# Kernel tuning notes

Measured on AMD Instinct MI355X. Metric: run time of the kernel, lower is better.

The kernel has to match this reference:

```python
import jax, jax.numpy as jnp
import numpy as np
from jax import lax

EPS = 1e-5


def binarize(x):
    return jnp.sign(x)


def conv3x3(x, w):
    # x: NCHW, w: OIHW, stride 1, padding 1 (SAME for k=3)
    return lax.conv_general_dilated(
        x, w, window_strides=(1, 1), padding=((1, 1), (1, 1)),
        dimension_numbers=("NCHW", "OIHW", "NCHW"))


def prelu(x, a):
    # a broadcastable per-channel slope
    return jnp.where(x >= 0, x, a * x)


def bn(x, gamma, beta, axes):
    mean = jnp.mean(x, axis=axes, keepdims=True)
    var = jnp.var(x, axis=axes, keepdims=True)
    shp = [1] * x.ndim
    shp[1] = x.shape[1]
    g = gamma.reshape(shp)
    b = beta.reshape(shp)
    return (x - mean) * lax.rsqrt(var + EPS) * g + b


def setup_inputs() -> dict:
    key = jax.random.key(0)
    ks = jax.random.split(key, 8)
    B = 256
    C = [1, 64, 128]
    FC_IN = 28 * 28 * C[-1]  # 100352
    F1, F2 = 1024, 10
    inp = {
        "x": jax.random.normal(ks[0], (B, C[0], 28, 28), jnp.float32),
        "cw0": jax.random.normal(ks[1], (C[1], C[0], 3, 3), jnp.float32) * 0.1,
        "cp0": jnp.full((C[1],), 0.25, jnp.float32),
        "cg0": jnp.ones((C[1],), jnp.float32),
        "cb0": jnp.zeros((C[1],), jnp.float32),
        "cw1": jax.random.normal(ks[2], (C[2], C[1], 3, 3), jnp.float32) * 0.1,
        "cp1": jnp.full((C[2],), 0.25, jnp.float32),
        "cg1": jnp.ones((C[2],), jnp.float32),
        "cb1": jnp.zeros((C[2],), jnp.float32),
        "fw0": jax.random.normal(ks[3], (F1, FC_IN), jnp.float32) * 0.02,
        "fp0": jnp.full((F1,), 0.25, jnp.float32),
        "fg0": jnp.ones((F1,), jnp.float32),
        "fb0": jnp.zeros((F1,), jnp.float32),
        "fw1": jax.random.normal(ks[4], (F2, F1), jnp.float32) * 0.05,
        "fp1": jnp.full((F2,), 0.25, jnp.float32),
        "fg1": jnp.ones((F2,), jnp.float32),
        "fb1": jnp.zeros((F2,), jnp.float32),
        "scale": jnp.ones((1,), jnp.float32),
    }
    return inp


def reference(x, cw0, cp0, cg0, cb0, cw1, cp1, cg1, cb1,
              fw0, fp0, fg0, fb0, fw1, fp1, fg1, fb1, scale):
    # conv block 0
    h = binarize(x)
    h = conv3x3(h, jnp.sign(cw0))
    h = prelu(h, cp0[None, :, None, None])
    h = bn(h, cg0, cb0, axes=(0, 2, 3))
    # conv block 1
    h = binarize(h)
    h = conv3x3(h, jnp.sign(cw1))
    h = prelu(h, cp1[None, :, None, None])
    h = bn(h, cg1, cb1, axes=(0, 2, 3))
    # flatten
    h = h.reshape(-1, 28 * 28 * cw1.shape[0])
    # fc block 0
    h = binarize(h)
    h = h @ jnp.sign(fw0).T
    h = prelu(h, fp0[None, :])
    h = bn(h, fg0, fb0, axes=(0,))
    # fc block 1
    h = binarize(h)
    h = h @ jnp.sign(fw1).T
    h = prelu(h, fp1[None, :])
    h = bn(h, fg1, fb1, axes=(0,))
    # scale layer
    return h * scale
```

## Files before the change

kernel.cpp:

```cpp
#include <hip/hip_runtime.h>
#include <stdint.h>


static constexpr int BATCH = 256;
static constexpr int C1    = 128;
static constexpr int K0    = 100352;
static constexpr int KW    = 1568;
static constexpr int N1    = 1024;
static constexpr int KS2   = 49;
static constexpr int JW2   = 32;
static constexpr int SUB2  = 8;
static constexpr int NS2   = 4;
static constexpr unsigned ZCAP = 65536;

__device__ __forceinline__ float fsign(float v){
    return (v > 0.f) ? 1.f : ((v < 0.f) ? -1.f : 0.f);
}

__global__ __launch_bounds__(256) void k_conv0(const float* __restrict__ x,
        const float* __restrict__ cw0, const float* __restrict__ cp0,
        int8_t* __restrict__ h0s, double* __restrict__ S0, double* __restrict__ Q0)
{
    __shared__ float img[30][30];
    __shared__ float redS[4][64];
    __shared__ float redQ[4][64];
    int b = blockIdx.x;
    int tid = threadIdx.x;
    for (int i = tid; i < 900; i += 256) ((float*)img)[i] = 0.f;
    __syncthreads();
    for (int i = tid; i < 784; i += 256) {
        float v = x[b*784 + i];
        img[1 + i/28][1 + i%28] = fsign(v);
    }
    __syncthreads();
    int lane = tid & 63, wv = tid >> 6;
    float wsg[9];
    #pragma unroll
    for (int t = 0; t < 9; t++) wsg[t] = fsign(cw0[lane*9 + t]);
    float a = cp0[lane];
    float accS = 0.f, accQ = 0.f;
    for (int i = 0; i < 196; i++) {
        int p = wv*196 + i;
        int y = p / 28, xx = p % 28;
        float s = 0.f;
        #pragma unroll
        for (int dy = 0; dy < 3; dy++)
            #pragma unroll
            for (int dx = 0; dx < 3; dx++)
                s += img[y+dy][xx+dx] * wsg[dy*3+dx];
        h0s[(size_t)(b*784 + p)*64 + lane] = (int8_t)(int)s;
        float v = (s >= 0.f) ? s : a*s;
        accS += v; accQ += v*v;
    }
    redS[wv][lane] = accS; redQ[wv][lane] = accQ;
    __syncthreads();
    if (tid < 64) {
        double s = (double)redS[0][tid] + redS[1][tid] + redS[2][tid] + redS[3][tid];
        double q = (double)redQ[0][tid] + redQ[1][tid] + redQ[2][tid] + redQ[3][tid];
        atomicAdd(&S0[tid], s);
        atomicAdd(&Q0[tid], q);
    }
}

__global__ void k_bnfin(const double* __restrict__ S, const double* __restrict__ Q,
        const float* __restrict__ g, const float* __restrict__ bb,
        double* __restrict__ AB, int C, double invN)
{
    int c = threadIdx.x;
    if (c >= C) return;
    double mean = S[c] * invN;
    double var  = Q[c] * invN - mean*mean;
    if (var < 0.0) var = 0.0;
    double A = (double)g[c] / sqrt(var + 1e-5);
    AB[c]     = A;
    AB[C + c] = (double)bb[c] - mean*A;
}

__global__ __launch_bounds__(256) void k_pack_h0(const int8_t* __restrict__ h0s,
        const float* __restrict__ cp0, const double* __restrict__ AB,
        uint64_t* __restrict__ hp)
{
    int idx = blockIdx.x * 4 + (threadIdx.x >> 6);
    int lane = threadIdx.x & 63;
    float s = (float)h0s[(size_t)idx*64 + lane];
    float a = cp0[lane];
    float v = (s >= 0.f) ? s : a*s;
    double t = fma((double)v, AB[lane], AB[64 + lane]);
    uint64_t m = __ballot(t < 0.0);
    if (lane == 0) hp[idx] = m;
}

__global__ __launch_bounds__(256) void k_pack_w1(const float* __restrict__ cw1,
        uint64_t* __restrict__ wn1, uint64_t* __restrict__ wnz1)
{
    int idx = blockIdx.x*4 + (threadIdx.x >> 6);
    int lane = threadIdx.x & 63;
    int oc = idx / 9, t = idx % 9;
    float w = cw1[oc*576 + lane*9 + t];
    uint64_t n = __ballot(w < 0.f);
    uint64_t z = __ballot(w != 0.f);
    if (lane == 0) { wn1[idx] = n; wnz1[idx] = z; }
}

__global__ __launch_bounds__(256) void k_conv1(const uint64_t* __restrict__ hp,
        const uint64_t* __restrict__ wn1, const uint64_t* __restrict__ wnz1,
        int16_t* __restrict__ h1s)
{
    int bid = blockIdx.x;
    int ocg = bid & 15;
    int ptg = (bid >> 4) & 3;
    int b   = bid >> 6;
    int wv = threadIdx.x >> 6, lane = threadIdx.x & 63;
    int pt = ptg*4 + wv;
    if (pt >= 13) return;
    int p = pt*64 + lane;
    bool pvalid = p < 784;
    int pcl = pvalid ? p : 783;
    int y = pcl / 28, xx = pcl % 28;
    uint64_t nb[9]; unsigned vmask = 0;
    #pragma unroll
    for (int dy = 0; dy < 3; dy++)
        #pragma unroll
        for (int dx = 0; dx < 3; dx++) {
            int t = dy*3+dx;
            int yy = y + dy - 1, xv = xx + dx - 1;
            bool ok = (yy >= 0 && yy < 28 && xv >= 0 && xv < 28);
            nb[t] = hp[b*784 + (ok ? (yy*28+xv) : 0)];
            if (ok) vmask |= 1u << t;
        }
    #pragma unroll
    for (int o = 0; o < 8; o++) {
        int oc = ocg*8 + o;
        int base = oc*9;
        int acc = 0;
        #pragma unroll
        for (int t = 0; t < 9; t++) {
            uint64_t wn = wn1[base+t], wz = wnz1[base+t];
            if (vmask & (1u<<t))
                acc += (int)__popcll(wz) - 2*(int)__popcll((nb[t] ^ wn) & wz);
        }
        if (pvalid) h1s[((size_t)b*128 + oc)*784 + p] = (int16_t)acc;
    }
}

__global__ __launch_bounds__(256) void k_stats1(const int16_t* __restrict__ h1s,
        const float* __restrict__ cp1, double* __restrict__ S1, double* __restrict__ Q1)
{
    int oc = blockIdx.x >> 3, bg = blockIdx.x & 7;
    int tid = threadIdx.x;
    float a = cp1[oc];
    float accS = 0.f, accQ = 0.f;
    for (int i = tid; i < 32*784; i += 256) {
        int b = bg*32 + i/784, p = i%784;
        float s = (float)h1s[((size_t)b*128+oc)*784 + p];
        float v = (s >= 0.f) ? s : a*s;
        accS += v; accQ += v*v;
    }
    __shared__ double rs[256], rq[256];
    rs[tid] = accS; rq[tid] = accQ;
    __syncthreads();
    for (int off = 128; off > 0; off >>= 1) {
        if (tid < off) { rs[tid] += rs[tid+off]; rq[tid] += rq[tid+off]; }
        __syncthreads();
    }
    if (tid == 0) { atomicAdd(&S1[oc], rs[0]); atomicAdd(&Q1[oc], rq[0]); }
}

__global__ __launch_bounds__(256) void k_pack_a0(const int16_t* __restrict__ h1s,
        const float* __restrict__ cp1, const double* __restrict__ AB,
        uint64_t* __restrict__ ap_t)
{
    int bb = blockIdx.x / 392;
    int jg = blockIdx.x % 392;
    int j = jg*4 + (threadIdx.x >> 6);
    int lane = threadIdx.x & 63;
    int k = j*64 + lane;
    int oc = k / 784;
    int p  = k - oc*784;
    float s = (float)h1s[((size_t)bb*128 + oc)*784 + p];
    float a = cp1[oc];
    float v = (s >= 0.f) ? s : a*s;
    double t = fma((double)v, AB[oc], AB[128+oc]);
    uint64_t m = __ballot(t < 0.0);
    if (lane == 0) ap_t[(size_t)j*256 + bb] = m;
}

__global__ __launch_bounds__(256) void k_pack_w0(const float* __restrict__ fw0,
        uint64_t* __restrict__ wp_t, unsigned* __restrict__ zcnt,
        uint64_t* __restrict__ zlist)
{
    int j = blockIdx.x;
    int wv = threadIdx.x >> 6, lane = threadIdx.x & 63;
    const float* col = fw0 + (size_t)j*64 + lane;
    int nbase = wv*256;
    for (int i = 0; i < 256; i += 4) {
        int n = nbase + i;
        float w0 = col[(size_t)(n+0)*K0];
        float w1 = col[(size_t)(n+1)*K0];
        float w2 = col[(size_t)(n+2)*K0];
        float w3 = col[(size_t)(n+3)*K0];
        uint64_t g0 = __ballot(w0 < 0.f), z0 = __ballot(w0 == 0.f);
        uint64_t g1 = __ballot(w1 < 0.f), z1 = __ballot(w1 == 0.f);
        uint64_t g2 = __ballot(w2 < 0.f), z2 = __ballot(w2 == 0.f);
        uint64_t g3 = __ballot(w3 < 0.f), z3 = __ballot(w3 == 0.f);
        if (lane == 0) {
            uint64_t* dst = wp_t + (size_t)j*N1 + n;
            dst[0] = g0; dst[1] = g1; dst[2] = g2; dst[3] = g3;
            uint64_t zs[4] = {z0, z1, z2, z3};
            #pragma unroll
            for (int r = 0; r < 4; r++) if (zs[r]) {
                unsigned id = atomicAdd(zcnt, 1u);
                if (id < ZCAP) {
                    zlist[2*id]   = ((uint64_t)(unsigned)(n+r) << 32) | (unsigned)j;
                    zlist[2*id+1] = zs[r];
                }
            }
        }
    }
}

__global__ __launch_bounds__(256) void k_fc0g(const uint64_t* __restrict__ wp_t,
        const uint64_t* __restrict__ ap_t, int16_t* __restrict__ pcpart)
{
    __shared__ uint64_t wL[SUB2][32];
    __shared__ uint64_t apL[SUB2][256];
    int nt = blockIdx.x & 31;
    int ks = blockIdx.x >> 5;
    int tid = threadIdx.x;
    int bq = tid & 31;
    int nq = tid >> 5;
    int n0 = nt*32;
    int pc[8][4];
    #pragma unroll
    for (int i=0;i<8;i++)
        #pragma unroll
        for (int k=0;k<4;k++) pc[i][k]=0;
    int jbase = ks*JW2;
    for (int c = 0; c < NS2; c++) {
        int j0 = jbase + c*SUB2;
        #pragma unroll
        for (int r = 0; r < SUB2; r++)
            apL[r][tid] = ap_t[(size_t)(j0 + r)*256 + tid];
        {
            int jj = tid >> 5, n = tid & 31;
            wL[jj][n] = wp_t[(size_t)(j0 + jj)*N1 + n0 + n];
        }
        __syncthreads();
        #pragma unroll
        for (int jj = 0; jj < SUB2; jj++) {
            uint64_t aw[8], ww[4];
            #pragma unroll
            for (int i = 0; i < 8; i++) aw[i] = apL[jj][bq + 32*i];
            #pragma unroll
            for (int k = 0; k < 4; k++) ww[k] = wL[jj][nq + 8*k];
            #pragma unroll
            for (int i = 0; i < 8; i++)
                #pragma unroll
                for (int k = 0; k < 4; k++)
                    pc[i][k] += (int)__popcll(aw[i] ^ ww[k]);
        }
        __syncthreads();
    }
    #pragma unroll
    for (int k = 0; k < 4; k++) {
        int n = n0 + nq + 8*k;
        #pragma unroll
        for (int i = 0; i < 8; i++)
            pcpart[((size_t)ks*N1 + n)*BATCH + (bq + 32*i)] = (int16_t)pc[i][k];
    }
}

__global__ __launch_bounds__(256) void k_corr(const unsigned* __restrict__ zcnt,
        const uint64_t* __restrict__ zlist, const uint64_t* __restrict__ ap_t,
        int* __restrict__ corr)
{
    unsigned cnt = *zcnt; if (cnt > ZCAP) cnt = ZCAP;
    int b = threadIdx.x;
    for (unsigned e = blockIdx.x; e < cnt; e += gridDim.x) {
        uint64_t key = zlist[2*e], zm = zlist[2*e+1];
        int n = (int)(key >> 32), j = (int)(key & 0xffffffffu);
        uint64_t a = ap_t[(size_t)j*256 + b];
        int c = 2*(int)__popcll(a & zm) - (int)__popcll(zm);
        atomicAdd(&corr[b*N1 + n], c);
    }
}

__global__ __launch_bounds__(256) void k_fc0ep(const int16_t* __restrict__ pcpart,
        const int* __restrict__ corr, const float* __restrict__ fp0,
        const float* __restrict__ fg0, const float* __restrict__ fb0,
        float* __restrict__ af)
{
    int n = blockIdx.x, b = threadIdx.x;
    int pc = 0;
    #pragma unroll
    for (int ks = 0; ks < KS2; ks++) pc += (int)pcpart[((size_t)ks*N1 + n)*BATCH + b];
    int s = K0 - 2*pc + corr[b*N1 + n];
    float a = fp0[n];
    float v = (s >= 0) ? (float)s : a*(float)s;
    __shared__ double rs[256], rq[256];
    rs[b] = v; rq[b] = (double)v*(double)v;
    __syncthreads();
    for (int off=128; off>0; off>>=1){
        if (b<off){ rs[b]+=rs[b+off]; rq[b]+=rq[b+off]; }
        __syncthreads();
    }
    __shared__ double AB[2];
    if (b == 0) {
        double mean = rs[0] / 256.0;
        double var = rq[0] / 256.0 - mean*mean;
        if (var < 0.0) var = 0.0;
        double A = (double)fg0[n] / sqrt(var + 1e-5);
        AB[0] = A; AB[1] = (double)fb0[n] - mean*A;
    }
    __syncthreads();
    double t = fma((double)v, AB[0], AB[1]);
    af[(size_t)n*256 + b] = (t > 0.0) ? 1.f : ((t < 0.0) ? -1.f : 0.f);
}

__global__ __launch_bounds__(256) void k_fc1a(const float* __restrict__ af,
        const float* __restrict__ fw1, float* __restrict__ part9)
{
    __shared__ float swL[10][32];
    int ks = blockIdx.x, b = threadIdx.x;
    for (int i = b; i < 320; i += 256) {
        int j = i / 32, kk = i % 32;
        swL[j][kk] = fsign(fw1[j*1024 + ks*32 + kk]);
    }
    __syncthreads();
    float acc[10];
    #pragma unroll
    for (int j=0;j<10;j++) acc[j]=0.f;
    for (int kk = 0; kk < 32; kk++) {
        float a = af[(size_t)(ks*32+kk)*256 + b];
        #pragma unroll
        for (int j=0;j<10;j++) acc[j] += a * swL[j][kk];
    }
    #pragma unroll
    for (int j=0;j<10;j++) part9[((size_t)ks*256 + b)*10 + j] = acc[j];
}

__global__ __launch_bounds__(256) void k_fc1b(const float* __restrict__ part9,
        const float* __restrict__ fp1, const float* __restrict__ fg1,
        const float* __restrict__ fb1, const float* __restrict__ scale,
        float* __restrict__ out)
{
    int b = threadIdx.x;
    float v[10];
    #pragma unroll
    for (int j=0;j<10;j++) v[j]=0.f;
    for (int ks=0; ks<32; ks++)
        #pragma unroll
        for (int j=0;j<10;j++) v[j] += part9[((size_t)ks*256+b)*10 + j];
    #pragma unroll
    for (int j=0;j<10;j++){
        float a = fp1[j];
        v[j] = (v[j] >= 0.f) ? v[j] : a*v[j];
    }
    __shared__ double sv[256];
    __shared__ double AB[2][10];
    for (int j=0;j<10;j++){
        sv[b] = (double)v[j];
        __syncthreads();
        for (int off=128;off>0;off>>=1){ if(b<off) sv[b]+=sv[b+off]; __syncthreads(); }
        double mean = sv[0]/256.0;
        __syncthreads();
        double d = (double)v[j]-mean;
        sv[b] = d*d;
        __syncthreads();
        for (int off=128;off>0;off>>=1){ if(b<off) sv[b]+=sv[b+off]; __syncthreads(); }
        if (b==0){
            double var = sv[0]/256.0;
            double A = (double)fg1[j]/sqrt(var+1e-5);
            AB[0][j]=A; AB[1][j]=(double)fb1[j] - mean*A;
        }
        __syncthreads();
    }
    float sc = scale[0];
    #pragma unroll
    for (int j=0;j<10;j++)
        out[b*10+j] = (float)fma((double)v[j], AB[0][j], AB[1][j]) * sc;
}

extern "C" void kernel_launch(void* const* d_in, const int* in_sizes, int n_in,
                              void* d_out, int out_size, void* d_ws, size_t ws_size,
                              hipStream_t stream)
{
    const float* x    = (const float*)d_in[0];
    const float* cw0  = (const float*)d_in[1];
    const float* cp0  = (const float*)d_in[2];
    const float* cg0  = (const float*)d_in[3];
    const float* cb0  = (const float*)d_in[4];
    const float* cw1  = (const float*)d_in[5];
    const float* cp1  = (const float*)d_in[6];
    const float* cg1  = (const float*)d_in[7];
    const float* cb1  = (const float*)d_in[8];
    const float* fw0  = (const float*)d_in[9];
    const float* fp0  = (const float*)d_in[10];
    const float* fg0  = (const float*)d_in[11];
    const float* fb0  = (const float*)d_in[12];
    const float* fw1  = (const float*)d_in[13];
    const float* fp1  = (const float*)d_in[14];
    const float* fg1  = (const float*)d_in[15];
    const float* fb1  = (const float*)d_in[16];
    const float* scale= (const float*)d_in[17];

    char* ws = (char*)d_ws;
    size_t off = 0;
    auto alloc = [&](size_t bytes)->char* {
        char* r = ws + off; off = (off + bytes + 255) & ~(size_t)255; return r; };

    double*   S0    = (double*)alloc(64*8);
    double*   Q0    = (double*)alloc(64*8);
    double*   S1    = (double*)alloc(128*8);
    double*   Q1    = (double*)alloc(128*8);
    unsigned* zcnt  = (unsigned*)alloc(256);
    int*      corr  = (int*)alloc((size_t)256*1024*4);
    size_t zero_bytes = off;
    double*   A0B0  = (double*)alloc(128*8);
    double*   A1B1  = (double*)alloc(256*8);
    int8_t*   h0s   = (int8_t*)alloc((size_t)256*784*64);
    uint64_t* hp    = (uint64_t*)alloc((size_t)256*784*8);
    int16_t*  h1s   = (int16_t*)alloc((size_t)256*128*784*2);
    uint64_t* ap_t  = (uint64_t*)alloc((size_t)KW*256*8);
    uint64_t* wn1   = (uint64_t*)alloc(1152*8);
    uint64_t* wnz1  = (uint64_t*)alloc(1152*8);
    uint64_t* wp_t  = (uint64_t*)alloc((size_t)KW*N1*8);
    int16_t*  pcpart= (int16_t*)alloc((size_t)KS2*N1*BATCH*2);
    float*    af    = (float*)alloc((size_t)1024*256*4);
    float*    part9 = (float*)alloc((size_t)32*256*10*4);
    uint64_t* zlist = (uint64_t*)alloc((size_t)ZCAP*16);
    (void)ws_size; (void)in_sizes; (void)n_in; (void)out_size;

    hipMemsetAsync(d_ws, 0, zero_bytes, stream);
    k_conv0  <<<256,    256, 0, stream>>>(x, cw0, cp0, h0s, S0, Q0);
    k_bnfin  <<<1,       64, 0, stream>>>(S0, Q0, cg0, cb0, A0B0, 64, 1.0/200704.0);
    k_pack_h0<<<50176, 256, 0, stream>>>(h0s, cp0, A0B0, hp);
    k_pack_w1<<<288,   256, 0, stream>>>(cw1, wn1, wnz1);
    k_conv1  <<<16384, 256, 0, stream>>>(hp, wn1, wnz1, h1s);
    k_stats1 <<<1024,  256, 0, stream>>>(h1s, cp1, S1, Q1);
    k_bnfin  <<<1,     128, 0, stream>>>(S1, Q1, cg1, cb1, A1B1, 128, 1.0/200704.0);
    k_pack_a0<<<100352,256, 0, stream>>>(h1s, cp1, A1B1, ap_t);
    k_pack_w0<<<KW,    256, 0, stream>>>(fw0, wp_t, zcnt, zlist);
    k_fc0g   <<<KS2*32,256, 0, stream>>>(wp_t, ap_t, pcpart);
    k_corr   <<<64,    256, 0, stream>>>(zcnt, zlist, ap_t, corr);
    k_fc0ep  <<<1024,  256, 0, stream>>>(pcpart, corr, fp0, fg0, fb0, af);
    k_fc1a   <<<32,    256, 0, stream>>>(af, fw1, part9);
    k_fc1b   <<<1,     256, 0, stream>>>(part9, fp1, fg1, fb1, scale, (float*)d_out);
}
```

Before: 428.8 us.

## Fuse conv1 BN stats, restructure fw0 packing, fold zero-weight correction into epilogue

```diff
diff --git a/kernel.cpp b/kernel.cpp
--- a/kernel.cpp
+++ b/kernel.cpp
@@ -3,7 +3,6 @@
 
 
 static constexpr int BATCH = 256;
-static constexpr int C1    = 128;
 static constexpr int K0    = 100352;
 static constexpr int KW    = 1568;
 static constexpr int N1    = 1024;
@@ -17,6 +16,11 @@
     return (v > 0.f) ? 1.f : ((v < 0.f) ? -1.f : 0.f);
 }
 
+__global__ void k_zero(int* __restrict__ p)
+{
+    p[threadIdx.x] = 0;
+}
+
 __global__ __launch_bounds__(256) void k_conv0(const float* __restrict__ x,
         const float* __restrict__ cw0, const float* __restrict__ cp0,
         int8_t* __restrict__ h0s, double* __restrict__ S0, double* __restrict__ Q0)
@@ -104,19 +108,21 @@
 
 __global__ __launch_bounds__(256) void k_conv1(const uint64_t* __restrict__ hp,
         const uint64_t* __restrict__ wn1, const uint64_t* __restrict__ wnz1,
-        int16_t* __restrict__ h1s)
-{
+        const float* __restrict__ cp1, int16_t* __restrict__ h1s,
+        double* __restrict__ S1, double* __restrict__ Q1)
+{
+    __shared__ float lS[4][8];
+    __shared__ float lQ[4][8];
     int bid = blockIdx.x;
     int ocg = bid & 15;
     int ptg = (bid >> 4) & 3;
     int b   = bid >> 6;
     int wv = threadIdx.x >> 6, lane = threadIdx.x & 63;
     int pt = ptg*4 + wv;
-    if (pt >= 13) return;
-    int p = pt*64 + lane;
-    bool pvalid = p < 784;
-    int pcl = pvalid ? p : 783;
-    int y = pcl / 28, xx = pcl % 28;
+    bool active = (pt < 13);
+    int p = active ? (pt*64 + lane) : 0;
+    bool pvalid = active && (p < 784);
+    int y = p / 28, xx = p % 28;
     uint64_t nb[9]; unsigned vmask = 0;
     #pragma unroll
     for (int dy = 0; dy < 3; dy++)
@@ -140,30 +146,24 @@
                 acc += (int)__popcll(wz) - 2*(int)__popcll((nb[t] ^ wn) & wz);
         }
         if (pvalid) h1s[((size_t)b*128 + oc)*784 + p] = (int16_t)acc;
-    }
-}
-
-__global__ __launch_bounds__(256) void k_stats1(const int16_t* __restrict__ h1s,
-        const float* __restrict__ cp1, double* __restrict__ S1, double* __restrict__ Q1)
-{
-    int oc = blockIdx.x >> 3, bg = blockIdx.x & 7;
-    int tid = threadIdx.x;
-    float a = cp1[oc];
-    float accS = 0.f, accQ = 0.f;
-    for (int i = tid; i < 32*784; i += 256) {
-        int b = bg*32 + i/784, p = i%784;
-        float s = (float)h1s[((size_t)b*128+oc)*784 + p];
-        float v = (s >= 0.f) ? s : a*s;
-        accS += v; accQ += v*v;
-    }
-    __shared__ double rs[256], rq[256];
-    rs[tid] = accS; rq[tid] = accQ;
-    __syncthreads();
-    for (int off = 128; off > 0; off >>= 1) {
-        if (tid < off) { rs[tid] += rs[tid+off]; rq[tid] += rq[tid+off]; }
-        __syncthreads();
-    }
-    if (tid == 0) { atomicAdd(&S1[oc], rs[0]); atomicAdd(&Q1[oc], rq[0]); }
+        float pr = cp1[oc];
+        float v = pvalid ? ((acc >= 0) ? (float)acc : pr*(float)acc) : 0.f;
+        float s = v, q = v*v;
+        #pragma unroll
+        for (int off = 32; off; off >>= 1) {
+            s += __shfl_xor(s, off);
+            q += __shfl_xor(q, off);
+        }
+        if (lane == 0) { lS[wv][o] = s; lQ[wv][o] = q; }
+    }
+    __syncthreads();
+    if (threadIdx.x < 8) {
+        int o = threadIdx.x;
+        double s = (double)lS[0][o] + lS[1][o] + lS[2][o] + lS[3][o];
+        double q = (double)lQ[0][o] + lQ[1][o] + lQ[2][o] + lQ[3][o];
+        atomicAdd(&S1[ocg*8 + o], s);
+        atomicAdd(&Q1[ocg*8 + o], q);
+    }
 }
 
 __global__ __launch_bounds__(256) void k_pack_a0(const int16_t* __restrict__ h1s,
@@ -189,30 +189,33 @@
         uint64_t* __restrict__ wp_t, unsigned* __restrict__ zcnt,
         uint64_t* __restrict__ zlist)
 {
-    int j = blockIdx.x;
+    int ng = blockIdx.x >> 3;
+    int ch = blockIdx.x & 7;
     int wv = threadIdx.x >> 6, lane = threadIdx.x & 63;
-    const float* col = fw0 + (size_t)j*64 + lane;
-    int nbase = wv*256;
-    for (int i = 0; i < 256; i += 4) {
-        int n = nbase + i;
-        float w0 = col[(size_t)(n+0)*K0];
-        float w1 = col[(size_t)(n+1)*K0];
-        float w2 = col[(size_t)(n+2)*K0];
-        float w3 = col[(size_t)(n+3)*K0];
-        uint64_t g0 = __ballot(w0 < 0.f), z0 = __ballot(w0 == 0.f);
-        uint64_t g1 = __ballot(w1 < 0.f), z1 = __ballot(w1 == 0.f);
-        uint64_t g2 = __ballot(w2 < 0.f), z2 = __ballot(w2 == 0.f);
-        uint64_t g3 = __ballot(w3 < 0.f), z3 = __ballot(w3 == 0.f);
+    int n0 = ng*8;
+    int jw0 = ch*196 + wv*49;
+    const float* base = fw0 + (size_t)n0*K0 + lane;
+    for (int t = 0; t < 49; ++t) {
+        int jw = jw0 + t;
+        size_t koff = (size_t)jw*64;
+        uint64_t nb[8], zb[8];
+        #pragma unroll
+        for (int r = 0; r < 8; ++r) {
+            float w = base[(size_t)r*K0 + koff];
+            nb[r] = __ballot(w < 0.f);
+            zb[r] = __ballot(w == 0.f);
+        }
+        uint64_t mine = nb[0];
+        #pragma unroll
+        for (int r = 1; r < 8; ++r) mine = (lane == r) ? nb[r] : mine;
+        if (lane < 8) wp_t[(size_t)jw*N1 + n0 + lane] = mine;
         if (lane == 0) {
-            uint64_t* dst = wp_t + (size_t)j*N1 + n;
-            dst[0] = g0; dst[1] = g1; dst[2] = g2; dst[3] = g3;
-            uint64_t zs[4] = {z0, z1, z2, z3};
             #pragma unroll
-            for (int r = 0; r < 4; r++) if (zs[r]) {
+            for (int r = 0; r < 8; ++r) if (zb[r]) {
                 unsigned id = atomicAdd(zcnt, 1u);
                 if (id < ZCAP) {
-                    zlist[2*id]   = ((uint64_t)(unsigned)(n+r) << 32) | (unsigned)j;
-                    zlist[2*id+1] = zs[r];
+                    zlist[2*id]   = ((uint64_t)(unsigned)(n0+r) << 32) | (unsigned)jw;
+                    zlist[2*id+1] = zb[r];
                 }
             }
         }
@@ -270,23 +273,9 @@
     }
 }
 
-__global__ __launch_bounds__(256) void k_corr(const unsigned* __restrict__ zcnt,
-        const uint64_t* __restrict__ zlist, const uint64_t* __restrict__ ap_t,
-        int* __restrict__ corr)
-{
-    unsigned cnt = *zcnt; if (cnt > ZCAP) cnt = ZCAP;
-    int b = threadIdx.x;
-    for (unsigned e = blockIdx.x; e < cnt; e += gridDim.x) {
-        uint64_t key = zlist[2*e], zm = zlist[2*e+1];
-        int n = (int)(key >> 32), j = (int)(key & 0xffffffffu);
-        uint64_t a = ap_t[(size_t)j*256 + b];
-        int c = 2*(int)__popcll(a & zm) - (int)__popcll(zm);
-        atomicAdd(&corr[b*N1 + n], c);
-    }
-}
-
 __global__ __launch_bounds__(256) void k_fc0ep(const int16_t* __restrict__ pcpart,
-        const int* __restrict__ corr, const float* __restrict__ fp0,
+        const unsigned* __restrict__ zcnt, const uint64_t* __restrict__ zlist,
+        const uint64_t* __restrict__ ap_t, const float* __restrict__ fp0,
         const float* __restrict__ fg0, const float* __restrict__ fb0,
         float* __restrict__ af)
 {
@@ -294,7 +283,16 @@
     int pc = 0;
     #pragma unroll
     for (int ks = 0; ks < KS2; ks++) pc += (int)pcpart[((size_t)ks*N1 + n)*BATCH + b];
-    int s = K0 - 2*pc + corr[b*N1 + n];
+    int s = K0 - 2*pc;
+    unsigned cnt = *zcnt; if (cnt > ZCAP) cnt = ZCAP;
+    for (unsigned e = 0; e < cnt; ++e) {
+        uint64_t key = zlist[2*e];
+        if ((int)(key >> 32) == n) {
+            uint64_t zm = zlist[2*e+1];
+            uint64_t a = ap_t[(size_t)(key & 0xffffffffu)*256 + b];
+            s += 2*(int)__popcll(a & zm) - (int)__popcll(zm);
+        }
+    }
     float a = fp0[n];
     float v = (s >= 0) ? (float)s : a*(float)s;
     __shared__ double rs[256], rq[256];
@@ -414,8 +412,6 @@
     double*   S1    = (double*)alloc(128*8);
     double*   Q1    = (double*)alloc(128*8);
     unsigned* zcnt  = (unsigned*)alloc(256);
-    int*      corr  = (int*)alloc((size_t)256*1024*4);
-    size_t zero_bytes = off;
     double*   A0B0  = (double*)alloc(128*8);
     double*   A1B1  = (double*)alloc(256*8);
     int8_t*   h0s   = (int8_t*)alloc((size_t)256*784*64);
@@ -431,19 +427,17 @@
     uint64_t* zlist = (uint64_t*)alloc((size_t)ZCAP*16);
     (void)ws_size; (void)in_sizes; (void)n_in; (void)out_size;
 
-    hipMemsetAsync(d_ws, 0, zero_bytes, stream);
-    k_conv0  <<<256,    256, 0, stream>>>(x, cw0, cp0, h0s, S0, Q0);
-    k_bnfin  <<<1,       64, 0, stream>>>(S0, Q0, cg0, cb0, A0B0, 64, 1.0/200704.0);
+    k_zero   <<<1,    1024, 0, stream>>>((int*)d_ws);
+    k_conv0  <<<256,   256, 0, stream>>>(x, cw0, cp0, h0s, S0, Q0);
+    k_bnfin  <<<1,      64, 0, stream>>>(S0, Q0, cg0, cb0, A0B0, 64, 1.0/200704.0);
     k_pack_h0<<<50176, 256, 0, stream>>>(h0s, cp0, A0B0, hp);
     k_pack_w1<<<288,   256, 0, stream>>>(cw1, wn1, wnz1);
-    k_conv1  <<<16384, 256, 0, stream>>>(hp, wn1, wnz1, h1s);
-    k_stats1 <<<1024,  256, 0, stream>>>(h1s, cp1, S1, Q1);
+    k_conv1  <<<16384, 256, 0, stream>>>(hp, wn1, wnz1, cp1, h1s, S1, Q1);
     k_bnfin  <<<1,     128, 0, stream>>>(S1, Q1, cg1, cb1, A1B1, 128, 1.0/200704.0);
     k_pack_a0<<<100352,256, 0, stream>>>(h1s, cp1, A1B1, ap_t);
-    k_pack_w0<<<KW,    256, 0, stream>>>(fw0, wp_t, zcnt, zlist);
+    k_pack_w0<<<1024,  256, 0, stream>>>(fw0, wp_t, zcnt, zlist);
     k_fc0g   <<<KS2*32,256, 0, stream>>>(wp_t, ap_t, pcpart);
-    k_corr   <<<64,    256, 0, stream>>>(zcnt, zlist, ap_t, corr);
-    k_fc0ep  <<<1024,  256, 0, stream>>>(pcpart, corr, fp0, fg0, fb0, af);
+    k_fc0ep  <<<1024,  256, 0, stream>>>(pcpart, zcnt, zlist, ap_t, fp0, fg0, fb0, af);
     k_fc1a   <<<32,    256, 0, stream>>>(af, fw1, part9);
     k_fc1b   <<<1,     256, 0, stream>>>(part9, fp1, fg1, fb1, scale, (float*)d_out);
 }
```

After: 403.8 us. 5.8% less time.
